# Kernel tuning notes

Hardware: AMD Instinct MI355X
Metric: run time of the kernel (lower is better)

Reference implementation:

```python
import jax, jax.numpy as jnp
import numpy as np

N = 100000
E = 3200000
IN_C = 256
HID = 64
OUT_C = 2
EPS = 1e-5


def setup_inputs() -> dict:
    key = jax.random.key(0)
    ks = jax.random.split(key, 8)
    x = jax.random.normal(ks[0], (N, IN_C), dtype=jnp.float32)
    edge_index = jax.random.randint(ks[1], (2, E), 0, N, dtype=jnp.int64)
    # GCNConv weights (PyG: out = A_hat @ (x W) + b)
    W1 = jax.random.normal(ks[2], (IN_C, HID), dtype=jnp.float32) / np.sqrt(IN_C)
    b1 = jnp.zeros((HID,), dtype=jnp.float32)
    W2 = jax.random.normal(ks[3], (HID, OUT_C), dtype=jnp.float32) / np.sqrt(HID)
    b2 = jnp.zeros((OUT_C,), dtype=jnp.float32)
    # BatchNorm affine params
    g1 = jnp.ones((HID,), dtype=jnp.float32)
    be1 = jnp.zeros((HID,), dtype=jnp.float32)
    g2 = jnp.ones((OUT_C,), dtype=jnp.float32)
    be2 = jnp.zeros((OUT_C,), dtype=jnp.float32)
    # Decoder linear
    Wd = jax.random.normal(ks[4], (OUT_C, IN_C), dtype=jnp.float32) / np.sqrt(OUT_C)
    bd = jnp.zeros((IN_C,), dtype=jnp.float32)
    return {"x": x, "edge_index": edge_index, "W1": W1, "b1": b1, "g1": g1,
            "be1": be1, "W2": W2, "b2": b2, "g2": g2, "be2": be2,
            "Wd": Wd, "bd": bd}


def gcn_conv(x, W, b, src, dst, n):
    # x: [N, Cin] -> [N, Cout]; symmetric-normalized aggregation with self-loops
    xw = x @ W  # [N, Cout]
    loops = jnp.arange(n, dtype=src.dtype)
    s = jnp.concatenate([src, loops])  # [E+N]
    d = jnp.concatenate([dst, loops])
    deg = jax.ops.segment_sum(jnp.ones_like(d, dtype=x.dtype), d, num_segments=n)
    dinv = jax.lax.rsqrt(deg)  # deg >= 1 thanks to self-loops
    norm = dinv[s] * dinv[d]   # [E+N]
    out = jax.ops.segment_sum(norm[:, None] * xw[s], d, num_segments=n)
    return out + b


def batch_norm(x, gamma, beta):
    # training-mode BN over node dim, biased variance (torch semantics)
    mu = jnp.mean(x, axis=0)
    var = jnp.mean(jnp.square(x - mu), axis=0)
    return (x - mu) * jax.lax.rsqrt(var + EPS) * gamma + beta


def reference(x, edge_index, W1, b1, g1, be1, W2, b2, g2, be2, Wd, bd):
    src, dst = edge_index[0], edge_index[1]
    n = x.shape[0]
    h = gcn_conv(x, W1, b1, src, dst, n)
    h = jax.nn.relu(batch_norm(h, g1, be1))
    # dropout: identity (inference)
    z = batch_norm(gcn_conv(h, W2, b2, src, dst, n), g2, be2)
    return z @ Wd + bd  # decoder: [N, IN_C]
```

## Files before the change

### kernel.cpp

```cpp
#include <hip/hip_runtime.h>
#include <hip/hip_bf16.h>

#define NN 100000
#define NE 3200000
#define INC 256
#define HID 64
#define OUTC 2
#define EPSV 1e-5f

#define SCAN_CHUNK 1024
#define NBLK ((NN + SCAN_CHUNK - 1) / SCAN_CHUNK)

#define NBUCK 128
#define BCAP  26000
#define BIN_CHUNK 4096
#define BIN_K 16
#define BIN_GRID ((NE + BIN_CHUNK - 1) / BIN_CHUNK)

#define NQUART 25000

typedef short short8 __attribute__((ext_vector_type(8)));
typedef float f32x4 __attribute__((ext_vector_type(4)));

static __device__ __forceinline__ float bf2f(unsigned short u) {
    return __uint_as_float((unsigned)u << 16);
}
static __device__ __forceinline__ unsigned short f2bf(float f) {
    __hip_bfloat16 hb = __float2bfloat16(f);
    return *(unsigned short*)&hb;
}

__global__ __launch_bounds__(256) void bin_kernel(const int* __restrict__ src,
                                                  const int* __restrict__ dst,
                                                  int* __restrict__ gtail,
                                                  int2* __restrict__ bbuf) {
    __shared__ int bcnt[NBUCK], bbase[NBUCK];
    int t = threadIdx.x;
    if (t < NBUCK) bcnt[t] = 0;
    __syncthreads();
    int base = blockIdx.x * BIN_CHUNK;
    int s[BIN_K], d[BIN_K], sl[BIN_K], bk[BIN_K];
#pragma unroll
    for (int r = 0; r < BIN_K; r++) {
        int i = base + r * 256 + t;
        bool v = i < NE;
        s[r] = v ? src[i] : 0;
        d[r] = v ? dst[i] : 0;
        bk[r] = (int)(((unsigned)d[r] * (unsigned)NBUCK) / (unsigned)NN);
        sl[r] = v ? atomicAdd(&bcnt[bk[r]], 1) : 0;
    }
    __syncthreads();
    if (t < NBUCK) bbase[t] = bcnt[t] ? atomicAdd(&gtail[t], bcnt[t]) : 0;
    __syncthreads();
#pragma unroll
    for (int r = 0; r < BIN_K; r++) {
        int i = base + r * 256 + t;
        if (i < NE) {
            int b = bk[r];
            bbuf[(size_t)b * BCAP + bbase[b] + sl[r]] = make_int2(s[r], d[r]);
        }
    }
}

__global__ __launch_bounds__(256) void hist2_kernel(const int2* __restrict__ bbuf,
                                                    const int* __restrict__ gtail,
                                                    int* __restrict__ cnt) {
    __shared__ int h[800];
    int b = blockIdx.x, t = threadIdx.x;
    int nb = (b * NN + NBUCK - 1) >> 7;
    int ne_ = ((b + 1) * NN + NBUCK - 1) >> 7;
    int range = ne_ - nb;
    for (int i = t; i < range; i += 256) h[i] = 0;
    __syncthreads();
    int ecnt = gtail[b];
    const int2* p = bbuf + (size_t)b * BCAP;
    for (int i = t; i < ecnt; i += 256) {
        int2 e = p[i];
        atomicAdd(&h[e.y - nb], 1);
    }
    __syncthreads();
    for (int i = t; i < range; i += 256) cnt[nb + i] = h[i];
}

__global__ void scan_btot_kernel(const int* __restrict__ cnt, int* __restrict__ btot) {
    __shared__ int red[4];
    int b = blockIdx.x, t = threadIdx.x;
    int base = b * SCAN_CHUNK;
    int v = 0;
    for (int j = t; j < SCAN_CHUNK; j += 256) {
        int idx = base + j;
        v += (idx < NN) ? cnt[idx] : 0;
    }
    for (int o = 32; o; o >>= 1) v += __shfl_xor(v, o);
    int wave = t >> 6, lane = t & 63;
    if (lane == 0) red[wave] = v;
    __syncthreads();
    if (t == 0) btot[b] = red[0] + red[1] + red[2] + red[3];
}

__global__ void scan_boff_kernel(const int* __restrict__ btot, int* __restrict__ boff) {
    __shared__ int wtot[2];
    int t = threadIdx.x;
    int lane = t & 63, wave = t >> 6;
    int v = (t < NBLK) ? btot[t] : 0;
    int s = v;
    for (int o = 1; o < 64; o <<= 1) {
        int u = __shfl_up(s, o);
        if (lane >= o) s += u;
    }
    if (lane == 63) wtot[wave] = s;
    __syncthreads();
    int add = (wave == 1) ? wtot[0] : 0;
    if (t < NBLK) boff[t] = s - v + add;
}

__global__ void scan_rowptr_kernel(const int* __restrict__ cnt, const int* __restrict__ boff,
                                   int* __restrict__ rowptr, float* __restrict__ dinv) {
    __shared__ int wsum[4];
    int b = blockIdx.x, t = threadIdx.x;
    int lane = t & 63, wave = t >> 6;
    int idx = b * SCAN_CHUNK + t * 4;
    int c0 = (idx + 0 < NN) ? cnt[idx + 0] : 0;
    int c1 = (idx + 1 < NN) ? cnt[idx + 1] : 0;
    int c2 = (idx + 2 < NN) ? cnt[idx + 2] : 0;
    int c3 = (idx + 3 < NN) ? cnt[idx + 3] : 0;
    int local = c0 + c1 + c2 + c3;
    int s = local;
    for (int o = 1; o < 64; o <<= 1) {
        int u = __shfl_up(s, o);
        if (lane >= o) s += u;
    }
    if (lane == 63) wsum[wave] = s;
    __syncthreads();
    if (t == 0) {
        int run = 0;
        for (int w = 0; w < 4; w++) { int x = wsum[w]; wsum[w] = run; run += x; }
    }
    __syncthreads();
    int start = boff[b] + wsum[wave] + (s - local);
    if (idx + 0 < NN) { rowptr[idx + 0] = start;                dinv[idx + 0] = rsqrtf((float)(c0 + 1)); }
    if (idx + 1 < NN) { rowptr[idx + 1] = start + c0;           dinv[idx + 1] = rsqrtf((float)(c1 + 1)); }
    if (idx + 2 < NN) { rowptr[idx + 2] = start + c0 + c1;      dinv[idx + 2] = rsqrtf((float)(c2 + 1)); }
    if (idx + 3 < NN) { rowptr[idx + 3] = start + c0 + c1 + c2; dinv[idx + 3] = rsqrtf((float)(c3 + 1)); }
    if (b == 0 && t == 0) rowptr[NN] = NE;
}

__global__ __launch_bounds__(256) void scatter2_kernel(const int2* __restrict__ bbuf,
                                                       const int* __restrict__ gtail,
                                                       const int* __restrict__ rowptr,
                                                       int* __restrict__ e_src) {
    __shared__ int fill[800];
    int b = blockIdx.x, t = threadIdx.x;
    int nb = (b * NN + NBUCK - 1) >> 7;
    int ne_ = ((b + 1) * NN + NBUCK - 1) >> 7;
    int range = ne_ - nb;
    for (int i = t; i < range; i += 256) fill[i] = 0;
    __syncthreads();
    int ecnt = gtail[b];
    const int2* p = bbuf + (size_t)b * BCAP;
    for (int i = t; i < ecnt; i += 256) {
        int2 e = p[i];
        int pos = rowptr[e.y] + atomicAdd(&fill[e.y - nb], 1);
        e_src[pos] = e.x;
    }
}

__global__ __launch_bounds__(256) void wprep_kernel(const float* __restrict__ W1,
                                                    unsigned short* __restrict__ Wtb) {
    int t = blockIdx.x * 256 + threadIdx.x;
    int c = t & 63;
    int k = t >> 6;
    Wtb[c * 256 + k] = f2bf(W1[k * 64 + c]);
}

#define G1_ROWS 32
#define LDP 264
__global__ __launch_bounds__(256) void gemm1_kernel(const float* __restrict__ x,
                                                    const unsigned short* __restrict__ Wtb,
                                                    const float* __restrict__ dinv,
                                                    unsigned short* __restrict__ xw1h) {
    __shared__ unsigned short xt[G1_ROWS * LDP];
    __shared__ unsigned short wt[HID * LDP];
    int t = threadIdx.x;
    size_t base = (size_t)blockIdx.x * G1_ROWS;

    const float4* xg = (const float4*)(x + base * INC);
#pragma unroll
    for (int ii = 0; ii < 8; ii++) {
        int idx4 = ii * 256 + t;
        float4 v = xg[idx4];
        int f = idx4 * 4;
        int row = f >> 8, k = f & 255;
        ushort4 u;
        u.x = f2bf(v.x); u.y = f2bf(v.y); u.z = f2bf(v.z); u.w = f2bf(v.w);
        *(ushort4*)(xt + row * LDP + k) = u;
    }
    const int4* wsrc = (const int4*)Wtb;
#pragma unroll
    for (int ii = 0; ii < 8; ii++) {
        int idx4 = ii * 256 + t;
        int4 v = wsrc[idx4];
        int e16 = idx4 * 8;
        int c = e16 >> 8, k = e16 & 255;
        *(int4*)(wt + c * LDP + k) = v;
    }
    __syncthreads();

    int lane = t & 63;
    int wave = t >> 6;
    int l15 = lane & 15;
    int hi = lane >> 4;
    int rgrp = wave & 1;
    int cgrp = wave >> 1;
    const unsigned short* ap = xt + (rgrp * 16 + l15) * LDP;
    const unsigned short* bp0 = wt + (cgrp * 32 + l15) * LDP;
    const unsigned short* bp1 = bp0 + 16 * LDP;
    f32x4 acc0 = {0.f, 0.f, 0.f, 0.f};
    f32x4 acc1 = {0.f, 0.f, 0.f, 0.f};
#pragma unroll
    for (int kk = 0; kk < 8; kk++) {
        int ko = kk * 32 + hi * 8;
        short8 a  = *(const short8*)(ap + ko);
        short8 b0 = *(const short8*)(bp0 + ko);
        short8 b1 = *(const short8*)(bp1 + ko);
        acc0 = __builtin_amdgcn_mfma_f32_16x16x32_bf16(a, b0, acc0, 0, 0, 0);
        acc1 = __builtin_amdgcn_mfma_f32_16x16x32_bf16(a, b1, acc1, 0, 0, 0);
    }
    unsigned short* ph = xw1h + (size_t)cgrp * NN * 32;
#pragma unroll
    for (int i = 0; i < 4; i++) {
        int grow = (int)base + rgrp * 16 + hi * 4 + i;
        float dv = dinv[grow];
        ph[(size_t)grow * 32 + l15]      = f2bf(acc0[i] * dv);
        ph[(size_t)grow * 32 + l15 + 16] = f2bf(acc1[i] * dv);
    }
}

__global__ __launch_bounds__(256) void agg1_kernel(const unsigned short* __restrict__ xw1h,
                                                   const int* __restrict__ rowptr,
                                                   const int* __restrict__ e_src,
                                                   const float* __restrict__ dinv,
                                                   const float* __restrict__ b1,
                                                   float* __restrict__ h1h,
                                                   float* __restrict__ sums1) {
    __shared__ float lsum[4][32], lsq[4][32];
    int t = threadIdx.x;
    int lane = t & 63;
    int wave = t >> 6;
    int grp = lane >> 3;
    int cl = lane & 7;
    int cohort = blockIdx.x & 7;
    int h = cohort & 1;
    int dq = cohort >> 1;
    const ushort4* plane = (const ushort4*)(xw1h + (size_t)h * NN * 32);
    float* hp = h1h + (size_t)h * NN * 32;
    float bb0 = b1[h * 32 + cl * 4 + 0];
    float bb1 = b1[h * 32 + cl * 4 + 1];
    float bb2 = b1[h * 32 + cl * 4 + 2];
    float bb3 = b1[h * 32 + cl * 4 + 3];
    int gid = ((blockIdx.x >> 3) * 4 + wave) * 8 + grp;
    int dlo = dq * NQUART;
    float ss0 = 0.f, ss1 = 0.f, ss2 = 0.f, ss3 = 0.f;
    float sq0 = 0.f, sq1 = 0.f, sq2 = 0.f, sq3 = 0.f;
    for (int d = dlo + gid; d < dlo + NQUART; d += 8192) {
        int beg = rowptr[d], end = rowptr[d + 1];
        float a0 = 0.f, a1 = 0.f, a2 = 0.f, a3 = 0.f;
        int e = beg;
        for (; e + 3 < end; e += 4) {
            int s0 = e_src[e], s1 = e_src[e + 1], s2 = e_src[e + 2], s3 = e_src[e + 3];
            ushort4 u0 = plane[(size_t)s0 * 8 + cl];
            ushort4 u1 = plane[(size_t)s1 * 8 + cl];
            ushort4 u2 = plane[(size_t)s2 * 8 + cl];
            ushort4 u3 = plane[(size_t)s3 * 8 + cl];
            a0 += bf2f(u0.x) + bf2f(u1.x) + bf2f(u2.x) + bf2f(u3.x);
            a1 += bf2f(u0.y) + bf2f(u1.y) + bf2f(u2.y) + bf2f(u3.y);
            a2 += bf2f(u0.z) + bf2f(u1.z) + bf2f(u2.z) + bf2f(u3.z);
            a3 += bf2f(u0.w) + bf2f(u1.w) + bf2f(u2.w) + bf2f(u3.w);
        }
        for (; e < end; e++) {
            int s = e_src[e];
            ushort4 u = plane[(size_t)s * 8 + cl];
            a0 += bf2f(u.x); a1 += bf2f(u.y); a2 += bf2f(u.z); a3 += bf2f(u.w);
        }
        ushort4 us = plane[(size_t)d * 8 + cl];
        a0 += bf2f(us.x); a1 += bf2f(us.y); a2 += bf2f(us.z); a3 += bf2f(us.w);
        float dv = dinv[d];
        float h0 = a0 * dv + bb0;
        float h1v = a1 * dv + bb1;
        float h2 = a2 * dv + bb2;
        float h3 = a3 * dv + bb3;
        f32x4 hv = {h0, h1v, h2, h3};
        *(f32x4*)(hp + (size_t)d * 32 + cl * 4) = hv;
        ss0 += h0; sq0 += h0 * h0;
        ss1 += h1v; sq1 += h1v * h1v;
        ss2 += h2; sq2 += h2 * h2;
        ss3 += h3; sq3 += h3 * h3;
    }
#pragma unroll
    for (int o = 8; o < 64; o <<= 1) {
        ss0 += __shfl_xor(ss0, o); sq0 += __shfl_xor(sq0, o);
        ss1 += __shfl_xor(ss1, o); sq1 += __shfl_xor(sq1, o);
        ss2 += __shfl_xor(ss2, o); sq2 += __shfl_xor(sq2, o);
        ss3 += __shfl_xor(ss3, o); sq3 += __shfl_xor(sq3, o);
    }
    if (grp == 0) {
        lsum[wave][cl * 4 + 0] = ss0; lsq[wave][cl * 4 + 0] = sq0;
        lsum[wave][cl * 4 + 1] = ss1; lsq[wave][cl * 4 + 1] = sq1;
        lsum[wave][cl * 4 + 2] = ss2; lsq[wave][cl * 4 + 2] = sq2;
        lsum[wave][cl * 4 + 3] = ss3; lsq[wave][cl * 4 + 3] = sq3;
    }
    __syncthreads();
    if (t < 32) {
        float S = lsum[0][t] + lsum[1][t] + lsum[2][t] + lsum[3][t];
        float Q = lsq[0][t] + lsq[1][t] + lsq[2][t] + lsq[3][t];
        atomicAdd(&sums1[h * 32 + t], S);
        atomicAdd(&sums1[64 + h * 32 + t], Q);
    }
}

__global__ __launch_bounds__(256) void gemm2_kernel(const float* __restrict__ h1h,
                                                    const float* __restrict__ sums1,
                                                    const float* __restrict__ g1,
                                                    const float* __restrict__ be1,
                                                    const float* __restrict__ W2,
                                                    const float* __restrict__ dinv,
                                                    float* __restrict__ xw2) {
    int lane = threadIdx.x & 63;
    int row = blockIdx.x * 4 + (threadIdx.x >> 6);
    if (row >= NN) return;
    int c = lane;
    const float invn = 1.0f / (float)NN;
    float mu = sums1[c] * invn;
    float var = sums1[64 + c] * invn - mu * mu;
    float sc = g1[c] * rsqrtf(var + EPSV);
    float sh = be1[c] - mu * sc;
    float hv = h1h[(size_t)(c >> 5) * NN * 32 + (size_t)row * 32 + (c & 31)] * sc + sh;
    hv = fmaxf(hv, 0.f);
    float p0 = hv * W2[c * 2 + 0];
    float p1 = hv * W2[c * 2 + 1];
    for (int o = 32; o; o >>= 1) {
        p0 += __shfl_xor(p0, o);
        p1 += __shfl_xor(p1, o);
    }
    if (lane == 0) {
        float dv = dinv[row];
        xw2[(size_t)row * 2 + 0] = p0 * dv;
        xw2[(size_t)row * 2 + 1] = p1 * dv;
    }
}

__global__ __launch_bounds__(256) void agg2_kernel(const float* __restrict__ xw2,
                                                   const int* __restrict__ rowptr,
                                                   const int* __restrict__ e_src,
                                                   const float* __restrict__ dinv,
                                                   const float* __restrict__ b2,
                                                   float* __restrict__ z2,
                                                   float* __restrict__ sums2) {
    __shared__ float red[4][4];
    int t = threadIdx.x;
    int lane = t & 63;
    int wave = t >> 6;
    int gl = lane & 7;
    int d = blockIdx.x * 32 + (t >> 3);
    int beg = rowptr[d], end = rowptr[d + 1];
    float a0 = 0.f, a1 = 0.f;
    int e = beg + gl;
    for (; e + 24 < end; e += 32) {
        int s0 = e_src[e], s1 = e_src[e + 8], s2 = e_src[e + 16], s3 = e_src[e + 24];
        float2 v0 = *(const float2*)(xw2 + (size_t)s0 * 2);
        float2 v1 = *(const float2*)(xw2 + (size_t)s1 * 2);
        float2 v2 = *(const float2*)(xw2 + (size_t)s2 * 2);
        float2 v3 = *(const float2*)(xw2 + (size_t)s3 * 2);
        a0 += v0.x + v1.x + v2.x + v3.x;
        a1 += v0.y + v1.y + v2.y + v3.y;
    }
    for (; e < end; e += 8) {
        int s = e_src[e];
        float2 v = *(const float2*)(xw2 + (size_t)s * 2);
        a0 += v.x;
        a1 += v.y;
    }
    if (gl == 0) {
        float2 sf = *(const float2*)(xw2 + (size_t)d * 2);
        a0 += sf.x;
        a1 += sf.y;
    }
    a0 += __shfl_xor(a0, 1); a1 += __shfl_xor(a1, 1);
    a0 += __shfl_xor(a0, 2); a1 += __shfl_xor(a1, 2);
    a0 += __shfl_xor(a0, 4); a1 += __shfl_xor(a1, 4);
    float dv = dinv[d];
    float z0 = a0 * dv + b2[0];
    float z1 = a1 * dv + b2[1];
    if (gl == 0) *(float2*)(z2 + (size_t)d * 2) = make_float2(z0, z1);
    float s0 = (gl == 0) ? z0 : 0.f;
    float s1 = (gl == 0) ? z1 : 0.f;
    float q0 = (gl == 0) ? z0 * z0 : 0.f;
    float q1 = (gl == 0) ? z1 * z1 : 0.f;
    for (int o = 8; o < 64; o <<= 1) {
        s0 += __shfl_xor(s0, o); s1 += __shfl_xor(s1, o);
        q0 += __shfl_xor(q0, o); q1 += __shfl_xor(q1, o);
    }
    if (lane == 0) { red[wave][0] = s0; red[wave][1] = s1; red[wave][2] = q0; red[wave][3] = q1; }
    __syncthreads();
    if (t < 4) {
        float v = red[0][t] + red[1][t] + red[2][t] + red[3][t];
        atomicAdd(&sums2[(blockIdx.x & 7) * 4 + t], v);
    }
}

__global__ __launch_bounds__(256) void decoder_kernel(const float* __restrict__ z2,
                                                      const float* __restrict__ sums2,
                                                      const float* __restrict__ g2,
                                                      const float* __restrict__ be2,
                                                      const float* __restrict__ Wd,
                                                      const float* __restrict__ bd,
                                                      float* __restrict__ out) {
    int g = blockIdx.x * 256 + threadIdx.x;
    int row = g >> 6;
    int c4 = (g & 63) * 4;
    float t0 = 0.f, t1 = 0.f, t2 = 0.f, t3 = 0.f;
#pragma unroll
    for (int bk = 0; bk < 8; bk++) {
        t0 += sums2[bk * 4 + 0]; t1 += sums2[bk * 4 + 1];
        t2 += sums2[bk * 4 + 2]; t3 += sums2[bk * 4 + 3];
    }
    const float invn = 1.0f / (float)NN;
    float mu0 = t0 * invn, mu1 = t1 * invn;
    float v0 = t2 * invn - mu0 * mu0;
    float v1 = t3 * invn - mu1 * mu1;
    float sc0 = g2[0] * rsqrtf(v0 + EPSV), sh0 = be2[0] - mu0 * sc0;
    float sc1 = g2[1] * rsqrtf(v1 + EPSV), sh1 = be2[1] - mu1 * sc1;
    float zb0 = z2[(size_t)row * 2 + 0] * sc0 + sh0;
    float zb1 = z2[(size_t)row * 2 + 1] * sc1 + sh1;
    float4 w0 = *(const float4*)(Wd + c4);
    float4 w1 = *(const float4*)(Wd + INC + c4);
    float4 bb = *(const float4*)(bd + c4);
    float4 o;
    o.x = zb0 * w0.x + zb1 * w1.x + bb.x;
    o.y = zb0 * w0.y + zb1 * w1.y + bb.y;
    o.z = zb0 * w0.z + zb1 * w1.z + bb.z;
    o.w = zb0 * w0.w + zb1 * w1.w + bb.w;
    *(float4*)(out + (size_t)row * INC + c4) = o;
}

static inline size_t align256(size_t x) { return (x + 255) & ~(size_t)255; }

extern "C" void kernel_launch(void* const* d_in, const int* in_sizes, int n_in,
                              void* d_out, int out_size, void* d_ws, size_t ws_size,
                              hipStream_t stream) {
    const float* x  = (const float*)d_in[0];
    const int*   ei = (const int*)d_in[1];
    const float* W1 = (const float*)d_in[2];
    const float* b1 = (const float*)d_in[3];
    const float* g1 = (const float*)d_in[4];
    const float* be1 = (const float*)d_in[5];
    const float* W2 = (const float*)d_in[6];
    const float* b2 = (const float*)d_in[7];
    const float* g2 = (const float*)d_in[8];
    const float* be2 = (const float*)d_in[9];
    const float* Wd = (const float*)d_in[10];
    const float* bd = (const float*)d_in[11];
    float* out = (float*)d_out;

    const int* src = ei;
    const int* dst = ei + NE;

    char* ws = (char*)d_ws;
    size_t off = 0;
    int* gtail = (int*)(ws + off);      off = align256(off + NBUCK * 4);
    float* sums1 = (float*)(ws + off);  off = align256(off + 128 * 4);
    float* sums2 = (float*)(ws + off);  off = align256(off + 32 * 4);
    size_t zero_bytes = off;
    int* cnt = (int*)(ws + off);        off = align256(off + NN * 4);
    int* rowptr = (int*)(ws + off);     off = align256(off + (NN + 1) * 4);
    float* dinv = (float*)(ws + off);   off = align256(off + NN * 4);
    int* btot = (int*)(ws + off);       off = align256(off + NBLK * 4);
    int* boff = (int*)(ws + off);       off = align256(off + NBLK * 4);
    unsigned short* Wtb = (unsigned short*)(ws + off); off = align256(off + (size_t)HID * INC * 2);
    int2* bbuf = (int2*)(ws + off);     off = align256(off + (size_t)NBUCK * BCAP * 8);
    int* e_src = (int*)(ws + off);      off = align256(off + (size_t)NE * 4 + 64);
    unsigned short* xw1h = (unsigned short*)(ws + off); off = align256(off + (size_t)NN * HID * 2);
    float* h1h = (float*)(ws + off);    off = align256(off + (size_t)NN * HID * 4);
    float* xw2 = (float*)(ws + off);    off = align256(off + (size_t)NN * 2 * 4);
    float* z2 = (float*)(ws + off);     off = align256(off + (size_t)NN * 2 * 4);
    (void)ws_size; (void)in_sizes; (void)n_in; (void)out_size;

    hipMemsetAsync(d_ws, 0, zero_bytes, stream);

    bin_kernel<<<BIN_GRID, 256, 0, stream>>>(src, dst, gtail, bbuf);
    hist2_kernel<<<NBUCK, 256, 0, stream>>>(bbuf, gtail, cnt);
    scan_btot_kernel<<<NBLK, 256, 0, stream>>>(cnt, btot);
    scan_boff_kernel<<<1, 128, 0, stream>>>(btot, boff);
    scan_rowptr_kernel<<<NBLK, 256, 0, stream>>>(cnt, boff, rowptr, dinv);
    scatter2_kernel<<<NBUCK, 256, 0, stream>>>(bbuf, gtail, rowptr, e_src);
    wprep_kernel<<<64, 256, 0, stream>>>(W1, Wtb);
    gemm1_kernel<<<NN / G1_ROWS, 256, 0, stream>>>(x, Wtb, dinv, xw1h);
    agg1_kernel<<<2048, 256, 0, stream>>>(xw1h, rowptr, e_src, dinv, b1, h1h, sums1);
    gemm2_kernel<<<(NN + 3) / 4, 256, 0, stream>>>(h1h, sums1, g1, be1, W2, dinv, xw2);
    agg2_kernel<<<NN * 8 / 256, 256, 0, stream>>>(xw2, rowptr, e_src, dinv, b2, z2, sums2);
    decoder_kernel<<<(NN * HID) / 256, 256, 0, stream>>>(z2, sums2, g2, be2, Wd, bd, out);
}
```

Baseline: 317.4 us.

## Split source nodes into halves so gather working set fits in cache

Each destination's edge list is now partitioned by whether the source node lies in the first or second half of the node range. The first-layer features are stored in four planes, split by source half and channel half. agg1 makes two passes, gathering only from one half's plane per pass, to shrink the random-gather working set and improve L2/MALL hit rates. The cost is an extra count array, more LDS and atomics in hist/scatter, and each thread holding four nodes' accumulators, which raises register pressure.

```diff
diff --git a/kernel.cpp b/kernel.cpp
--- a/kernel.cpp
+++ b/kernel.cpp
@@ -18,6 +18,7 @@
 #define BIN_GRID ((NE + BIN_CHUNK - 1) / BIN_CHUNK)
 
 #define NQUART 25000
+#define SHALF 50000
 
 typedef short short8 __attribute__((ext_vector_type(8)));
 typedef float f32x4 __attribute__((ext_vector_type(4)));
@@ -64,22 +65,25 @@
 
 __global__ __launch_bounds__(256) void hist2_kernel(const int2* __restrict__ bbuf,
                                                     const int* __restrict__ gtail,
-                                                    int* __restrict__ cnt) {
-    __shared__ int h[800];
+                                                    int* __restrict__ cnt,
+                                                    int* __restrict__ cnt0) {
+    __shared__ int h[800], h0[800];
     int b = blockIdx.x, t = threadIdx.x;
     int nb = (b * NN + NBUCK - 1) >> 7;
     int ne_ = ((b + 1) * NN + NBUCK - 1) >> 7;
     int range = ne_ - nb;
-    for (int i = t; i < range; i += 256) h[i] = 0;
+    for (int i = t; i < range; i += 256) { h[i] = 0; h0[i] = 0; }
     __syncthreads();
     int ecnt = gtail[b];
     const int2* p = bbuf + (size_t)b * BCAP;
     for (int i = t; i < ecnt; i += 256) {
         int2 e = p[i];
-        atomicAdd(&h[e.y - nb], 1);
-    }
-    __syncthreads();
-    for (int i = t; i < range; i += 256) cnt[nb + i] = h[i];
+        int loc = e.y - nb;
+        atomicAdd(&h[loc], 1);
+        if (e.x < SHALF) atomicAdd(&h0[loc], 1);
+    }
+    __syncthreads();
+    for (int i = t; i < range; i += 256) { cnt[nb + i] = h[i]; cnt0[nb + i] = h0[i]; }
 }
 
 __global__ void scan_btot_kernel(const int* __restrict__ cnt, int* __restrict__ btot) {
@@ -148,19 +152,29 @@
 __global__ __launch_bounds__(256) void scatter2_kernel(const int2* __restrict__ bbuf,
                                                        const int* __restrict__ gtail,
                                                        const int* __restrict__ rowptr,
+                                                       const int* __restrict__ cnt0,
                                                        int* __restrict__ e_src) {
-    __shared__ int fill[800];
+    __shared__ int rp[800], mid[800], f0[800], f1[800];
     int b = blockIdx.x, t = threadIdx.x;
     int nb = (b * NN + NBUCK - 1) >> 7;
     int ne_ = ((b + 1) * NN + NBUCK - 1) >> 7;
     int range = ne_ - nb;
-    for (int i = t; i < range; i += 256) fill[i] = 0;
+    for (int i = t; i < range; i += 256) {
+        int r = rowptr[nb + i];
+        rp[i] = r;
+        mid[i] = r + cnt0[nb + i];
+        f0[i] = 0;
+        f1[i] = 0;
+    }
     __syncthreads();
     int ecnt = gtail[b];
     const int2* p = bbuf + (size_t)b * BCAP;
     for (int i = t; i < ecnt; i += 256) {
         int2 e = p[i];
-        int pos = rowptr[e.y] + atomicAdd(&fill[e.y - nb], 1);
+        int loc = e.y - nb;
+        int pos;
+        if (e.x < SHALF) pos = rp[loc] + atomicAdd(&f0[loc], 1);
+        else             pos = mid[loc] + atomicAdd(&f1[loc], 1);
         e_src[pos] = e.x;
     }
 }
@@ -178,7 +192,7 @@
 __global__ __launch_bounds__(256) void gemm1_kernel(const float* __restrict__ x,
                                                     const unsigned short* __restrict__ Wtb,
                                                     const float* __restrict__ dinv,
-                                                    unsigned short* __restrict__ xw1h) {
+                                                    unsigned short* __restrict__ xw1s) {
     __shared__ unsigned short xt[G1_ROWS * LDP];
     __shared__ unsigned short wt[HID * LDP];
     int t = threadIdx.x;
@@ -226,18 +240,21 @@
         acc0 = __builtin_amdgcn_mfma_f32_16x16x32_bf16(a, b0, acc0, 0, 0, 0);
         acc1 = __builtin_amdgcn_mfma_f32_16x16x32_bf16(a, b1, acc1, 0, 0, 0);
     }
-    unsigned short* ph = xw1h + (size_t)cgrp * NN * 32;
 #pragma unroll
     for (int i = 0; i < 4; i++) {
         int grow = (int)base + rgrp * 16 + hi * 4 + i;
         float dv = dinv[grow];
-        ph[(size_t)grow * 32 + l15]      = f2bf(acc0[i] * dv);
-        ph[(size_t)grow * 32 + l15 + 16] = f2bf(acc1[i] * dv);
-    }
-}
-
-__global__ __launch_bounds__(256) void agg1_kernel(const unsigned short* __restrict__ xw1h,
+        int sh = grow >= SHALF;
+        unsigned short* ph = xw1s + ((size_t)(sh * 2 + cgrp)) * SHALF * 32
+                                  + (size_t)(grow - sh * SHALF) * 32;
+        ph[l15]      = f2bf(acc0[i] * dv);
+        ph[l15 + 16] = f2bf(acc1[i] * dv);
+    }
+}
+
+__global__ __launch_bounds__(256) void agg1_kernel(const unsigned short* __restrict__ xw1s,
                                                    const int* __restrict__ rowptr,
+                                                   const int* __restrict__ cnt0,
                                                    const int* __restrict__ e_src,
                                                    const float* __restrict__ dinv,
                                                    const float* __restrict__ b1,
@@ -249,53 +266,91 @@
     int wave = t >> 6;
     int grp = lane >> 3;
     int cl = lane & 7;
-    int cohort = blockIdx.x & 7;
-    int h = cohort & 1;
-    int dq = cohort >> 1;
-    const ushort4* plane = (const ushort4*)(xw1h + (size_t)h * NN * 32);
-    float* hp = h1h + (size_t)h * NN * 32;
-    float bb0 = b1[h * 32 + cl * 4 + 0];
-    float bb1 = b1[h * 32 + cl * 4 + 1];
-    float bb2 = b1[h * 32 + cl * 4 + 2];
-    float bb3 = b1[h * 32 + cl * 4 + 3];
+    int c = blockIdx.x & 7;
+    int chH = c & 1;
+    int dq = c >> 1;
+    float* hp = h1h + (size_t)chH * NN * 32;
+    float bb0 = b1[chH * 32 + cl * 4 + 0];
+    float bb1 = b1[chH * 32 + cl * 4 + 1];
+    float bb2 = b1[chH * 32 + cl * 4 + 2];
+    float bb3 = b1[chH * 32 + cl * 4 + 3];
     int gid = ((blockIdx.x >> 3) * 4 + wave) * 8 + grp;
-    int dlo = dq * NQUART;
+    int dlo = dq * NQUART, dhi = dlo + NQUART;
+
+    int dn0 = dlo + gid, dn1 = dn0 + 8192, dn2 = dn1 + 8192, dn3 = dn2 + 8192;
+    int b0_ = 0, m0_ = 0, e0_ = 0, b1_ = 0, m1_ = 0, e1_ = 0;
+    int b2_ = 0, m2_ = 0, e2_ = 0, b3_ = 0, m3_ = 0, e3_ = 0;
+    if (dn0 < dhi) { b0_ = rowptr[dn0]; e0_ = rowptr[dn0 + 1]; m0_ = b0_ + cnt0[dn0]; }
+    if (dn1 < dhi) { b1_ = rowptr[dn1]; e1_ = rowptr[dn1 + 1]; m1_ = b1_ + cnt0[dn1]; }
+    if (dn2 < dhi) { b2_ = rowptr[dn2]; e2_ = rowptr[dn2 + 1]; m2_ = b2_ + cnt0[dn2]; }
+    if (dn3 < dhi) { b3_ = rowptr[dn3]; e3_ = rowptr[dn3 + 1]; m3_ = b3_ + cnt0[dn3]; }
+
+    float ac0[4] = {0.f, 0.f, 0.f, 0.f};
+    float ac1[4] = {0.f, 0.f, 0.f, 0.f};
+    float ac2[4] = {0.f, 0.f, 0.f, 0.f};
+    float ac3[4] = {0.f, 0.f, 0.f, 0.f};
+
+#pragma unroll
+    for (int pass = 0; pass < 2; pass++) {
+        const ushort4* plane = (const ushort4*)(xw1s + ((size_t)(pass * 2 + chH)) * SHALF * 32);
+        int sbase = pass * SHALF;
+#define AGG_NODE(DN, BV, MV, EV, AC)                                            \
+        if (DN < dhi) {                                                         \
+            int beg = pass ? MV : BV;                                           \
+            int end = pass ? EV : MV;                                           \
+            float a0 = 0.f, a1 = 0.f, a2 = 0.f, a3 = 0.f;                       \
+            int e = beg;                                                        \
+            for (; e + 3 < end; e += 4) {                                       \
+                int s0 = e_src[e] - sbase, s1 = e_src[e + 1] - sbase;           \
+                int s2 = e_src[e + 2] - sbase, s3 = e_src[e + 3] - sbase;       \
+                ushort4 u0 = plane[(size_t)s0 * 8 + cl];                        \
+                ushort4 u1 = plane[(size_t)s1 * 8 + cl];                        \
+                ushort4 u2 = plane[(size_t)s2 * 8 + cl];                        \
+                ushort4 u3 = plane[(size_t)s3 * 8 + cl];                        \
+                a0 += bf2f(u0.x) + bf2f(u1.x) + bf2f(u2.x) + bf2f(u3.x);        \
+                a1 += bf2f(u0.y) + bf2f(u1.y) + bf2f(u2.y) + bf2f(u3.y);        \
+                a2 += bf2f(u0.z) + bf2f(u1.z) + bf2f(u2.z) + bf2f(u3.z);        \
+                a3 += bf2f(u0.w) + bf2f(u1.w) + bf2f(u2.w) + bf2f(u3.w);        \
+            }                                                                   \
+            for (; e < end; e++) {                                              \
+                int s = e_src[e] - sbase;                                       \
+                ushort4 u = plane[(size_t)s * 8 + cl];                          \
+                a0 += bf2f(u.x); a1 += bf2f(u.y); a2 += bf2f(u.z); a3 += bf2f(u.w); \
+            }                                                                   \
+            AC[0] += a0; AC[1] += a1; AC[2] += a2; AC[3] += a3;                 \
+        }
+        AGG_NODE(dn0, b0_, m0_, e0_, ac0)
+        AGG_NODE(dn1, b1_, m1_, e1_, ac1)
+        AGG_NODE(dn2, b2_, m2_, e2_, ac2)
+        AGG_NODE(dn3, b3_, m3_, e3_, ac3)
+#undef AGG_NODE
+    }
+
     float ss0 = 0.f, ss1 = 0.f, ss2 = 0.f, ss3 = 0.f;
     float sq0 = 0.f, sq1 = 0.f, sq2 = 0.f, sq3 = 0.f;
-    for (int d = dlo + gid; d < dlo + NQUART; d += 8192) {
-        int beg = rowptr[d], end = rowptr[d + 1];
-        float a0 = 0.f, a1 = 0.f, a2 = 0.f, a3 = 0.f;
-        int e = beg;
-        for (; e + 3 < end; e += 4) {
-            int s0 = e_src[e], s1 = e_src[e + 1], s2 = e_src[e + 2], s3 = e_src[e + 3];
-            ushort4 u0 = plane[(size_t)s0 * 8 + cl];
-            ushort4 u1 = plane[(size_t)s1 * 8 + cl];
-            ushort4 u2 = plane[(size_t)s2 * 8 + cl];
-            ushort4 u3 = plane[(size_t)s3 * 8 + cl];
-            a0 += bf2f(u0.x) + bf2f(u1.x) + bf2f(u2.x) + bf2f(u3.x);
-            a1 += bf2f(u0.y) + bf2f(u1.y) + bf2f(u2.y) + bf2f(u3.y);
-            a2 += bf2f(u0.z) + bf2f(u1.z) + bf2f(u2.z) + bf2f(u3.z);
-            a3 += bf2f(u0.w) + bf2f(u1.w) + bf2f(u2.w) + bf2f(u3.w);
-        }
-        for (; e < end; e++) {
-            int s = e_src[e];
-            ushort4 u = plane[(size_t)s * 8 + cl];
-            a0 += bf2f(u.x); a1 += bf2f(u.y); a2 += bf2f(u.z); a3 += bf2f(u.w);
-        }
-        ushort4 us = plane[(size_t)d * 8 + cl];
-        a0 += bf2f(us.x); a1 += bf2f(us.y); a2 += bf2f(us.z); a3 += bf2f(us.w);
-        float dv = dinv[d];
-        float h0 = a0 * dv + bb0;
-        float h1v = a1 * dv + bb1;
-        float h2 = a2 * dv + bb2;
-        float h3 = a3 * dv + bb3;
-        f32x4 hv = {h0, h1v, h2, h3};
-        *(f32x4*)(hp + (size_t)d * 32 + cl * 4) = hv;
-        ss0 += h0; sq0 += h0 * h0;
-        ss1 += h1v; sq1 += h1v * h1v;
-        ss2 += h2; sq2 += h2 * h2;
-        ss3 += h3; sq3 += h3 * h3;
-    }
+#define FIN_NODE(DN, AC)                                                        \
+    if (DN < dhi) {                                                             \
+        int sh = DN >= SHALF;                                                   \
+        const ushort4* sp = (const ushort4*)(xw1s + ((size_t)(sh * 2 + chH)) * SHALF * 32); \
+        ushort4 us = sp[(size_t)(DN - sh * SHALF) * 8 + cl];                    \
+        float dv = dinv[DN];                                                    \
+        float h0 = (AC[0] + bf2f(us.x)) * dv + bb0;                             \
+        float h1v = (AC[1] + bf2f(us.y)) * dv + bb1;                            \
+        float h2 = (AC[2] + bf2f(us.z)) * dv + bb2;                             \
+        float h3 = (AC[3] + bf2f(us.w)) * dv + bb3;                             \
+        f32x4 hv = {h0, h1v, h2, h3};                                           \
+        *(f32x4*)(hp + (size_t)DN * 32 + cl * 4) = hv;                          \
+        ss0 += h0; sq0 += h0 * h0;                                              \
+        ss1 += h1v; sq1 += h1v * h1v;                                           \
+        ss2 += h2; sq2 += h2 * h2;                                              \
+        ss3 += h3; sq3 += h3 * h3;                                              \
+    }
+    FIN_NODE(dn0, ac0)
+    FIN_NODE(dn1, ac1)
+    FIN_NODE(dn2, ac2)
+    FIN_NODE(dn3, ac3)
+#undef FIN_NODE
+
 #pragma unroll
     for (int o = 8; o < 64; o <<= 1) {
         ss0 += __shfl_xor(ss0, o); sq0 += __shfl_xor(sq0, o);
@@ -313,8 +368,8 @@
     if (t < 32) {
         float S = lsum[0][t] + lsum[1][t] + lsum[2][t] + lsum[3][t];
         float Q = lsq[0][t] + lsq[1][t] + lsq[2][t] + lsq[3][t];
-        atomicAdd(&sums1[h * 32 + t], S);
-        atomicAdd(&sums1[64 + h * 32 + t], Q);
+        atomicAdd(&sums1[chH * 32 + t], S);
+        atomicAdd(&sums1[64 + chH * 32 + t], Q);
     }
 }
 
@@ -472,6 +527,7 @@
     float* sums2 = (float*)(ws + off);  off = align256(off + 32 * 4);
     size_t zero_bytes = off;
     int* cnt = (int*)(ws + off);        off = align256(off + NN * 4);
+    int* cnt0 = (int*)(ws + off);       off = align256(off + NN * 4);
     int* rowptr = (int*)(ws + off);     off = align256(off + (NN + 1) * 4);
     float* dinv = (float*)(ws + off);   off = align256(off + NN * 4);
     int* btot = (int*)(ws + off);       off = align256(off + NBLK * 4);
@@ -479,7 +535,7 @@
     unsigned short* Wtb = (unsigned short*)(ws + off); off = align256(off + (size_t)HID * INC * 2);
     int2* bbuf = (int2*)(ws + off);     off = align256(off + (size_t)NBUCK * BCAP * 8);
     int* e_src = (int*)(ws + off);      off = align256(off + (size_t)NE * 4 + 64);
-    unsigned short* xw1h = (unsigned short*)(ws + off); off = align256(off + (size_t)NN * HID * 2);
+    unsigned short* xw1s = (unsigned short*)(ws + off); off = align256(off + (size_t)NN * HID * 2);
     float* h1h = (float*)(ws + off);    off = align256(off + (size_t)NN * HID * 4);
     float* xw2 = (float*)(ws + off);    off = align256(off + (size_t)NN * 2 * 4);
     float* z2 = (float*)(ws + off);     off = align256(off + (size_t)NN * 2 * 4);
@@ -488,14 +544,14 @@
     hipMemsetAsync(d_ws, 0, zero_bytes, stream);
 
     bin_kernel<<<BIN_GRID, 256, 0, stream>>>(src, dst, gtail, bbuf);
-    hist2_kernel<<<NBUCK, 256, 0, stream>>>(bbuf, gtail, cnt);
+    hist2_kernel<<<NBUCK, 256, 0, stream>>>(bbuf, gtail, cnt, cnt0);
     scan_btot_kernel<<<NBLK, 256, 0, stream>>>(cnt, btot);
     scan_boff_kernel<<<1, 128, 0, stream>>>(btot, boff);
     scan_rowptr_kernel<<<NBLK, 256, 0, stream>>>(cnt, boff, rowptr, dinv);
-    scatter2_kernel<<<NBUCK, 256, 0, stream>>>(bbuf, gtail, rowptr, e_src);
+    scatter2_kernel<<<NBUCK, 256, 0, stream>>>(bbuf, gtail, rowptr, cnt0, e_src);
     wprep_kernel<<<64, 256, 0, stream>>>(W1, Wtb);
-    gemm1_kernel<<<NN / G1_ROWS, 256, 0, stream>>>(x, Wtb, dinv, xw1h);
-    agg1_kernel<<<2048, 256, 0, stream>>>(xw1h, rowptr, e_src, dinv, b1, h1h, sums1);
+    gemm1_kernel<<<NN / G1_ROWS, 256, 0, stream>>>(x, Wtb, dinv, xw1s);
+    agg1_kernel<<<2048, 256, 0, stream>>>(xw1s, rowptr, cnt0, e_src, dinv, b1, h1h, sums1);
     gemm2_kernel<<<(NN + 3) / 4, 256, 0, stream>>>(h1h, sums1, g1, be1, W2, dinv, xw2);
     agg2_kernel<<<NN * 8 / 256, 256, 0, stream>>>(xw2, rowptr, e_src, dinv, b2, z2, sums2);
     decoder_kernel<<<(NN * HID) / 256, 256, 0, stream>>>(z2, sums2, g2, be2, Wd, bd, out);
```

Result: no change. 323.7 us (+2.0%).
